# Kernel tuning notes

Measured on AMD Instinct MI355X. Metric: run time of the kernel, lower is better.

## Reference

```python
import jax, jax.numpy as jnp
import numpy as np

B, IN, H, T = 4096, 1024, 1024, 12
TIME_PENALTY = 0.01
PONDER_EPS = 0.01


def lstm_cell(x, h, c, Wih, Whh, bih, bhh):
    # PyTorch LSTMCell: gates ordered i, f, g, o
    g = x @ Wih.T + bih + h @ Whh.T + bhh  # [B, 4H]
    i, f, gg, o = jnp.split(g, 4, axis=1)
    i = jax.nn.sigmoid(i)
    f = jax.nn.sigmoid(f)
    gg = jnp.tanh(gg)
    o = jax.nn.sigmoid(o)
    c_new = f * c + i * gg
    h_new = o * jnp.tanh(c_new)
    return h_new, c_new


def setup_inputs() -> dict:
    key = jax.random.key(0)
    ks = jax.random.split(key, 12)
    k1 = 1.0 / np.sqrt(H)
    u = lambda k, shape: jax.random.uniform(k, shape, jnp.float32, -k1, k1)
    return {
        "inputs": jax.random.normal(ks[0], (B, IN), jnp.float32),
        "W_ih1": u(ks[1], (4 * H, IN + 1)),
        "W_hh1": u(ks[2], (4 * H, H)),
        "b_ih1": u(ks[3], (4 * H,)),
        "b_hh1": u(ks[4], (4 * H,)),
        "W_ih2": u(ks[5], (4 * H, H)),
        "W_hh2": u(ks[6], (4 * H, H)),
        "b_ih2": u(ks[7], (4 * H,)),
        "b_hh2": u(ks[8], (4 * H,)),
        "W_halt": u(ks[9], (1, H)),
        "b_halt": jnp.full((1,), -1.0, jnp.float32),  # initial_halting_bias
    }


def reference(inputs, W_ih1, W_hh1, b_ih1, b_hh1, W_ih2, W_hh2, b_ih2, b_hh2, W_halt, b_halt):
    batch = inputs.shape[0]
    budget = jnp.float32(1.0 - PONDER_EPS)

    h1 = jnp.zeros((batch, H), jnp.float32)
    c1 = jnp.zeros((batch, H), jnp.float32)
    h2 = jnp.zeros((batch, H), jnp.float32)
    c2 = jnp.zeros((batch, H), jnp.float32)
    halt_accum = jnp.zeros((batch, 1), jnp.float32)
    acc_out = jnp.zeros((batch, H), jnp.float32)
    acc_rem = jnp.zeros((batch, 1), jnp.float32)
    ponder_steps = jnp.zeros((batch,), jnp.float32)
    cont = jnp.ones((batch, 1), bool)
    is_first = jnp.array(True)

    def step(carry, _):
        h1, c1, h2, c2, halt_accum, acc_out, acc_rem, ponder_steps, cont, is_first = carry
        active = jnp.any(cont)  # mimic torch's early break: inactive steps are no-ops
        flag = jnp.where(is_first, 1.0, 0.0) * jnp.ones((batch, 1), jnp.float32)
        x = jnp.concatenate([inputs, flag], axis=1)
        h1n, c1n = lstm_cell(x, h1, c1, W_ih1, W_hh1, b_ih1, b_hh1)
        act = jax.nn.relu(h1n)
        h2n, c2n = lstm_cell(act, h2, c2, W_ih2, W_hh2, b_ih2, b_hh2)
        step_halt = jax.nn.sigmoid(h2n @ W_halt.T + b_halt)  # [B,1]
        cont_f = cont.astype(jnp.float32)
        masked_halt = step_halt * cont_f
        halt_n = halt_accum + masked_halt
        ending = (halt_n > budget) & cont
        cont_n = cont & jnp.logical_not(ending)
        masked_rem = ending.astype(jnp.float32) * (1.0 - halt_n)
        acc_out_n = acc_out + (masked_halt + masked_rem) * h2n
        acc_rem_n = acc_rem + masked_halt
        ponder_n = ponder_steps + cont_n[:, 0].astype(jnp.float32)
        sel = lambda new, old: jnp.where(active, new, old)
        carry_n = (sel(h1n, h1), sel(c1n, c1), sel(h2n, h2), sel(c2n, c2),
                   sel(halt_n, halt_accum), sel(acc_out_n, acc_out),
                   sel(acc_rem_n, acc_rem), sel(ponder_n, ponder_steps),
                   jnp.where(active, cont_n, cont),
                   is_first & jnp.logical_not(active))
        return carry_n, None

    carry = (h1, c1, h2, c2, halt_accum, acc_out, acc_rem, ponder_steps, cont, is_first)
    carry, _ = jax.lax.scan(step, carry, None, length=T)
    h1, c1, h2, c2, halt_accum, acc_out, acc_rem, ponder_steps, cont, _ = carry

    # for-else branch: samples still continuing after time_limit get the remainder
    acc_out = acc_out + cont.astype(jnp.float32) * (1.0 - halt_accum) * h2
    ponder_cost = -1.0 * TIME_PENALTY * jnp.mean(acc_rem)
    return acc_out, h1, c1, h2, c2, ponder_cost, ponder_steps
```

## Files before the change

kernel.cpp:

```cpp
#include <hip/hip_runtime.h>
#include <cstdint>
#include <cstddef>


typedef _Float16 f16;
typedef f16   f16x8 __attribute__((ext_vector_type(8)));
typedef f16   f16x4 __attribute__((ext_vector_type(4)));
typedef float f32x4 __attribute__((ext_vector_type(4)));

#define TSTEPS 12

#define O_ACC   0u
#define O_H1    4194304u
#define O_C1    8388608u
#define O_H2    12582912u
#define O_C2    16777216u
#define O_PCOST 20971520u
#define O_PSTEP 20971521u
#define DO_W1HI (16u<<20)
#define DO_W1LO (24u<<20)
#define DO_W2HI (32u<<20)
#define DO_W2LO (40u<<20)
#define DO_W3HI (48u<<20)
#define DO_W3LO (56u<<20)
#define DO_XHI  (64u<<20)
#define DO_XLO  (72u<<20)

#define WS_C1    (size_t)(0u)
#define WS_C2    ((size_t)16u<<20)
#define WS_H1HI0 ((size_t)32u<<20)
#define WS_H1HI1 ((size_t)40u<<20)
#define WS_H1LO0 ((size_t)48u<<20)
#define WS_H1LO1 ((size_t)56u<<20)
#define WS_H2HI0 ((size_t)64u<<20)
#define WS_H2HI1 ((size_t)72u<<20)
#define WS_H2LO0 ((size_t)80u<<20)
#define WS_H2LO1 ((size_t)88u<<20)
#define WS_ACTHI ((size_t)96u<<20)
#define WS_ACTLO ((size_t)104u<<20)
#define WS_MISC  ((size_t)112u<<20)

#define OFF_AHI 0
#define OFF_ALO 16384
#define OFF_BHI 32768
#define OFF_BLO 49152

__device__ __forceinline__ float sigmoidf_(float x) { return 1.0f / (1.0f + expf(-x)); }

__device__ __forceinline__ void glds16(const void* g, void* l) {
    __builtin_amdgcn_global_load_lds(
        (const __attribute__((address_space(1))) unsigned int*)g,
        (__attribute__((address_space(3))) unsigned int*)l, 16, 0, 0);
}

__device__ __forceinline__ void tile_compute(char* sm, f32x4 (&acc)[4][4],
                                             int wr0, int cs, int l15, int lk)
{
#pragma unroll
    for (int ks = 0; ks < 2; ++ks) {
        f16x8 ah[4], al[4];
#pragma unroll
        for (int mf = 0; mf < 4; ++mf) {
            const int row = wr0 + mf * 16 + l15;
            const int off = row * 128 + ((((ks << 2) + lk) ^ (row & 7)) << 4);
            ah[mf] = *(const f16x8*)(sm + OFF_AHI + off);
            al[mf] = *(const f16x8*)(sm + OFF_ALO + off);
        }
#pragma unroll
        for (int g = 0; g < 4; ++g) {
            const int lv  = cs * 64 + g * 16 + l15;
            const int off = lv * 128 + ((((ks << 2) + lk) ^ (lv & 7)) << 4);
            const f16x8 bh = *(const f16x8*)(sm + OFF_BHI + off);
            const f16x8 bl = *(const f16x8*)(sm + OFF_BLO + off);
#pragma unroll
            for (int mf = 0; mf < 4; ++mf) {
                acc[mf][g] = __builtin_amdgcn_mfma_f32_16x16x32_f16(ah[mf], bh, acc[mf][g], 0, 0, 0);
                acc[mf][g] = __builtin_amdgcn_mfma_f32_16x16x32_f16(ah[mf], bl, acc[mf][g], 0, 0, 0);
                acc[mf][g] = __builtin_amdgcn_mfma_f32_16x16x32_f16(al[mf], bh, acc[mf][g], 0, 0, 0);
            }
        }
    }
}

__device__ __forceinline__ void pass_glds(
    const f16* __restrict__ Ahi, const f16* __restrict__ Alo,
    const f16* __restrict__ Bhi, const f16* __restrict__ Blo,
    int m0, int hc0, f32x4 (&acc)[4][4], char* sm, bool first)
{
    const int tid = threadIdx.x, lane = tid & 63, wid = tid >> 6;
    const int wr0 = (wid >> 1) * 64, cs = wid & 1, l15 = lane & 15, lk = lane >> 4;
    const int rl = lane >> 3, sl = lane & 7;
    const int swz = (sl ^ rl) << 3;

    const f16* gsrc;
    int lbase;
    if (wid == 0)      { gsrc = Ahi + (size_t)(m0 + rl) * 1024 + swz; lbase = OFF_AHI; }
    else if (wid == 1) { gsrc = Alo + (size_t)(m0 + rl) * 1024 + swz; lbase = OFF_ALO; }
    else if (wid == 2) { gsrc = Bhi + (size_t)(hc0 + rl) * 1024 + swz; lbase = OFF_BHI; }
    else               { gsrc = Blo + (size_t)(hc0 + rl) * 1024 + swz; lbase = OFF_BLO; }

    for (int kt = 0; kt < 16; ++kt) {
        if (!first || kt) __syncthreads();
        const f16* g = gsrc + kt * 64;
        if (wid < 2) {
#pragma unroll
            for (int i = 0; i < 16; ++i)
                glds16(g + (size_t)i * 8192, sm + lbase + i * 1024);
        } else {
#pragma unroll
            for (int i = 0; i < 16; ++i) {
                const size_t rowoff =
                    (size_t)(((i >> 1) & 3) * 1024 + (i >> 3) * 16 + (i & 1) * 8) * 1024;
                glds16(g + rowoff, sm + lbase + i * 1024);
            }
        }
        __syncthreads();
        tile_compute(sm, acc, wr0, cs, l15, lk);
    }
}

__device__ __forceinline__ void pass_mixed(
    const f16* __restrict__ Ahi, const f16* __restrict__ Alo,
    const float* __restrict__ Bw,
    int m0, int hc0, f32x4 (&acc)[4][4], char* sm, bool first)
{
    const int tid = threadIdx.x, lane = tid & 63, wid = tid >> 6;
    const int wr0 = (wid >> 1) * 64, cs = wid & 1, l15 = lane & 15, lk = lane >> 4;
    const int rl = lane >> 3, sl = lane & 7;
    const int swz = (sl ^ rl) << 3;
    const f16* gsrc = (wid == 0 ? Ahi : Alo) + (size_t)(m0 + rl) * 1024 + swz;
    const int lbase = (wid == 0) ? OFF_AHI : OFF_ALO;

    const int blv = tid >> 1, bkh = (tid & 1) << 5;
    const int brow = ((blv >> 4) & 3) * 1024 + hc0 + (blv >> 6) * 16 + (blv & 15);
    const float* bsrc = Bw + (size_t)brow * 1024 + bkh;

    float4 bv[8];
    auto loadB = [&](int kt) {
#pragma unroll
        for (int i = 0; i < 8; ++i) bv[i] = *(const float4*)(bsrc + kt * 64 + i * 4);
    };
    auto writeB = [&]() {
#pragma unroll
        for (int i = 0; i < 8; ++i) {
            const float4 v = bv[i];
            const f16 s0 = (f16)v.x, s1 = (f16)v.y, s2 = (f16)v.z, s3 = (f16)v.w;
            const f16x4 hv = {s0, s1, s2, s3};
            const f16x4 lw = {(f16)(v.x - (float)s0), (f16)(v.y - (float)s1),
                              (f16)(v.z - (float)s2), (f16)(v.w - (float)s3)};
            const int kslot = (tid & 1) * 4 + (i >> 1);
            const int off = blv * 128 + ((kslot ^ (blv & 7)) << 4) + (i & 1) * 8;
            *(f16x4*)(sm + OFF_BHI + off) = hv;
            *(f16x4*)(sm + OFF_BLO + off) = lw;
        }
    };

    loadB(0);
    for (int kt = 0; kt < 16; ++kt) {
        if (!first || kt) __syncthreads();
        if (wid < 2) {
            const f16* g = gsrc + kt * 64;
#pragma unroll
            for (int i = 0; i < 16; ++i)
                glds16(g + (size_t)i * 8192, sm + lbase + i * 1024);
        }
        writeB();
        __syncthreads();
        if (kt < 15) loadB(kt + 1);
        tile_compute(sm, acc, wr0, cs, l15, lk);
    }
}

__device__ __forceinline__ void block_tile(int& m0, int& hc0) {
    const int bid = blockIdx.x;
    const int lid = (bid & 7) * 128 + (bid >> 3);
    m0  = (lid & 31) * 128;
    hc0 = (lid >> 5) * 32;
}

__global__ __launch_bounds__(256) void k_stepA(
    const f16* __restrict__ xhi, const f16* __restrict__ xlo,
    const f16* __restrict__ W1hi, const f16* __restrict__ W1lo,
    const float* __restrict__ Whh1,
    const f16* __restrict__ h1hi_in, const f16* __restrict__ h1lo_in,
    const float* __restrict__ bih1, const float* __restrict__ bhh1,
    const float* __restrict__ flagcol,
    float* __restrict__ c1,
    f16* __restrict__ h1hi_out, f16* __restrict__ h1lo_out,
    f16* __restrict__ acthi, f16* __restrict__ actlo,
    const unsigned* __restrict__ cnt_prev, int step)
{
    if (step > 0 && cnt_prev[0] == 0u) return;
    __shared__ __align__(16) char sm[65536];
    int m0, hc0; block_tile(m0, hc0);
    f32x4 acc[4][4];
#pragma unroll
    for (int a = 0; a < 4; ++a)
#pragma unroll
        for (int b = 0; b < 4; ++b) acc[a][b] = (f32x4){0.f, 0.f, 0.f, 0.f};

    pass_glds(xhi, xlo, W1hi, W1lo, m0, hc0, acc, sm, true);
    if (step > 0)
        pass_mixed(h1hi_in, h1lo_in, Whh1, m0, hc0, acc, sm, false);

    const int tid = threadIdx.x, lane = tid & 63, wid = tid >> 6;
    const int wr0 = (wid >> 1) * 64, cs = wid & 1, l15 = lane & 15, lk = lane >> 4;
#pragma unroll
    for (int mf = 0; mf < 4; ++mf)
#pragma unroll
        for (int r = 0; r < 4; ++r) {
            const int row = m0 + wr0 + mf * 16 + lk * 4 + r;
            const int hc  = hc0 + cs * 16 + l15;
            float p[4];
#pragma unroll
            for (int g = 0; g < 4; ++g) {
                const int R = g * 1024 + hc;
                p[g] = acc[mf][g][r] + bih1[R] + bhh1[R];
                if (step == 0) p[g] += flagcol[R];
            }
            const float ig = sigmoidf_(p[0]);
            const float fg = sigmoidf_(p[1]);
            const float gg = tanhf(p[2]);
            const float og = sigmoidf_(p[3]);
            const int idx = row * 1024 + hc;
            const float cn = fg * c1[idx] + ig * gg;
            c1[idx] = cn;
            const float h = og * tanhf(cn);
            const f16 hh = (f16)h;
            const f16 hl = (f16)(h - (float)hh);
            h1hi_out[idx] = hh; h1lo_out[idx] = hl;
            const bool pos = h > 0.0f;
            acthi[idx] = pos ? hh : (f16)0.0f;
            actlo[idx] = pos ? hl : (f16)0.0f;
        }
}

__global__ __launch_bounds__(256) void k_stepB(
    const f16* __restrict__ acthi, const f16* __restrict__ actlo,
    const f16* __restrict__ W2hi, const f16* __restrict__ W2lo,
    const f16* __restrict__ h2hi_in, const f16* __restrict__ h2lo_in,
    const f16* __restrict__ W3hi, const f16* __restrict__ W3lo,
    const float* __restrict__ bih2, const float* __restrict__ bhh2,
    float* __restrict__ c2, f16* __restrict__ h2hi_out, f16* __restrict__ h2lo_out,
    const unsigned* __restrict__ cnt_prev, int step)
{
    if (step > 0 && cnt_prev[0] == 0u) return;
    __shared__ __align__(16) char sm[65536];
    int m0, hc0; block_tile(m0, hc0);
    f32x4 acc[4][4];
#pragma unroll
    for (int a = 0; a < 4; ++a)
#pragma unroll
        for (int b = 0; b < 4; ++b) acc[a][b] = (f32x4){0.f, 0.f, 0.f, 0.f};

    pass_glds(acthi, actlo, W2hi, W2lo, m0, hc0, acc, sm, true);
    if (step > 0)
        pass_glds(h2hi_in, h2lo_in, W3hi, W3lo, m0, hc0, acc, sm, false);

    const int tid = threadIdx.x, lane = tid & 63, wid = tid >> 6;
    const int wr0 = (wid >> 1) * 64, cs = wid & 1, l15 = lane & 15, lk = lane >> 4;
#pragma unroll
    for (int mf = 0; mf < 4; ++mf)
#pragma unroll
        for (int r = 0; r < 4; ++r) {
            const int row = m0 + wr0 + mf * 16 + lk * 4 + r;
            const int hc  = hc0 + cs * 16 + l15;
            float p[4];
#pragma unroll
            for (int g = 0; g < 4; ++g) {
                const int R = g * 1024 + hc;
                p[g] = acc[mf][g][r] + bih2[R] + bhh2[R];
            }
            const float ig = sigmoidf_(p[0]);
            const float fg = sigmoidf_(p[1]);
            const float gg = tanhf(p[2]);
            const float og = sigmoidf_(p[3]);
            const int idx = row * 1024 + hc;
            const float cn = fg * c2[idx] + ig * gg;
            c2[idx] = cn;
            const float h = og * tanhf(cn);
            const f16 hh = (f16)h;
            h2hi_out[idx] = hh;
            h2lo_out[idx] = (f16)(h - (float)hh);
        }
}

__global__ __launch_bounds__(256) void k_halt(
    const f16* __restrict__ h2hi, const f16* __restrict__ h2lo,
    const float* __restrict__ Whalt, const float* __restrict__ bhalt,
    float* __restrict__ halt, float* __restrict__ cont, float* __restrict__ coef,
    float* __restrict__ ponder_out, unsigned* __restrict__ ctrl,
    const unsigned* __restrict__ cnt_prev, int step)
{
    if (step > 0 && cnt_prev[0] == 0u) return;
    const int lane = threadIdx.x & 63;
    const int b = blockIdx.x * 4 + (threadIdx.x >> 6);
    const size_t base = (size_t)b * 1024;
    float sum = 0.0f;
    for (int k = lane; k < 1024; k += 64)
        sum += ((float)h2hi[base + k] + (float)h2lo[base + k]) * Whalt[k];
#pragma unroll
    for (int off = 32; off > 0; off >>= 1) sum += __shfl_down(sum, off, 64);
    if (lane == 0) {
        const float sh = sigmoidf_(sum + bhalt[0]);
        float co = 0.0f;
        if (cont[b] != 0.0f) {
            const float hn = halt[b] + sh;
            const bool ending = hn > 0.99f;
            co = sh + (ending ? (1.0f - hn) : 0.0f);
            halt[b] = hn;
            if (!ending) {
                ponder_out[b] += 1.0f;
                atomicAdd(&ctrl[step], 1u);
            } else {
                cont[b] = 0.0f;
            }
        }
        coef[b] = co;
        if (b == 0) ctrl[12] = (unsigned)(step + 1);
    }
}

__global__ __launch_bounds__(256) void k_accum(
    const f16* __restrict__ h2hi, const f16* __restrict__ h2lo,
    const float* __restrict__ coef, float* __restrict__ acc_out,
    const unsigned* __restrict__ cnt_prev, int step)
{
    if (step > 0 && cnt_prev[0] == 0u) return;
    const int b = blockIdx.x;
    const float co = coef[b];
    if (co == 0.0f) return;
    const size_t base = (size_t)b * 1024;
    const int i = threadIdx.x;
    const f16x4 hv = *(const f16x4*)(h2hi + base + i * 4);
    const f16x4 lv = *(const f16x4*)(h2lo + base + i * 4);
    float4* dst = (float4*)(acc_out + base);
    float4 d = dst[i];
    d.x = fmaf(co, (float)hv[0] + (float)lv[0], d.x);
    d.y = fmaf(co, (float)hv[1] + (float)lv[1], d.y);
    d.z = fmaf(co, (float)hv[2] + (float)lv[2], d.z);
    d.w = fmaf(co, (float)hv[3] + (float)lv[3], d.w);
    dst[i] = d;
}

__global__ __launch_bounds__(256) void k_small_init(
    float* __restrict__ halt, float* __restrict__ cont,
    float* __restrict__ ponder_out, unsigned* __restrict__ ctrl)
{
    const int b = blockIdx.x * 256 + threadIdx.x;
    if (b < 4096) { halt[b] = 0.0f; cont[b] = 1.0f; ponder_out[b] = 0.0f; }
    if (b < 16) ctrl[b] = 0u;
}

__global__ __launch_bounds__(256) void k_split_flat(
    const float* __restrict__ src, f16* __restrict__ hi, f16* __restrict__ lo)
{
    const size_t i = ((size_t)blockIdx.x * 256 + threadIdx.x) * 4;
    const float4 v = *(const float4*)(src + i);
    const f16 s0 = (f16)v.x, s1 = (f16)v.y, s2 = (f16)v.z, s3 = (f16)v.w;
    const f16x4 hv = {s0, s1, s2, s3};
    const f16x4 lw = {(f16)(v.x - (float)s0), (f16)(v.y - (float)s1),
                      (f16)(v.z - (float)s2), (f16)(v.w - (float)s3)};
    *(f16x4*)(hi + i) = hv;
    *(f16x4*)(lo + i) = lw;
}

__global__ __launch_bounds__(256) void k_split_wih1(
    const float* __restrict__ src, f16* __restrict__ hi, f16* __restrict__ lo,
    float* __restrict__ flagcol)
{
    const int t = blockIdx.x * 256 + threadIdx.x;
    const int row = t >> 8, c4 = (t & 255) << 2;
    const float* s = src + (size_t)row * 1025 + c4;
    const float v0 = s[0], v1 = s[1], v2 = s[2], v3 = s[3];
    const f16 s0 = (f16)v0, s1 = (f16)v1, s2 = (f16)v2, s3 = (f16)v3;
    const f16x4 hv = {s0, s1, s2, s3};
    const f16x4 lw = {(f16)(v0 - (float)s0), (f16)(v1 - (float)s1),
                      (f16)(v2 - (float)s2), (f16)(v3 - (float)s3)};
    const size_t di = (size_t)row * 1024 + c4;
    *(f16x4*)(hi + di) = hv;
    *(f16x4*)(lo + di) = lw;
    if ((t & 255) == 0) flagcol[row] = src[(size_t)row * 1025 + 1024];
}

__global__ __launch_bounds__(256) void k_fin1(
    const f16* __restrict__ h1hi0, const f16* __restrict__ h1hi1,
    const f16* __restrict__ h1lo0, const f16* __restrict__ h1lo1,
    const f16* __restrict__ h2hi0, const f16* __restrict__ h2hi1,
    const f16* __restrict__ h2lo0, const f16* __restrict__ h2lo1,
    const float* __restrict__ c1s, const float* __restrict__ c2s,
    const float* __restrict__ halt, const float* __restrict__ cont,
    const unsigned* __restrict__ ctrl, float* __restrict__ out)
{
    const int par = (int)(ctrl[12] & 1u);
    const f16* h1h = par ? h1hi1 : h1hi0;
    const f16* h1l = par ? h1lo1 : h1lo0;
    const f16* h2h = par ? h2hi1 : h2hi0;
    const f16* h2l = par ? h2lo1 : h2lo0;
    const int b = blockIdx.x;
    const float rem = (cont[b] != 0.0f) ? (1.0f - halt[b]) : 0.0f;
    const int base = b * 1024;
    for (int i = threadIdx.x; i < 1024; i += 256) {
        const float h1v = (float)h1h[base + i] + (float)h1l[base + i];
        const float h2v = (float)h2h[base + i] + (float)h2l[base + i];
        out[O_H1 + base + i] = h1v;
        out[O_C1 + base + i] = c1s[base + i];
        out[O_H2 + base + i] = h2v;
        out[O_C2 + base + i] = c2s[base + i];
        if (rem != 0.0f) out[O_ACC + base + i] += rem * h2v;
    }
}

__global__ __launch_bounds__(256) void k_fin2(
    const float* __restrict__ halt, float* __restrict__ out)
{
    __shared__ float red[256];
    float s = 0.0f;
    for (int i = threadIdx.x; i < 4096; i += 256) s += halt[i];
    red[threadIdx.x] = s;
    __syncthreads();
    for (int w = 128; w > 0; w >>= 1) {
        if (threadIdx.x < w) red[threadIdx.x] += red[threadIdx.x + w];
        __syncthreads();
    }
    if (threadIdx.x == 0) out[O_PCOST] = -0.01f * (red[0] * (1.0f / 4096.0f));
}

extern "C" void kernel_launch(void* const* d_in, const int* in_sizes, int n_in,
                              void* d_out, int out_size, void* d_ws, size_t ws_size,
                              hipStream_t stream) {
    const float* inputs = (const float*)d_in[0];
    const float* W_ih1  = (const float*)d_in[1];
    const float* W_hh1  = (const float*)d_in[2];
    const float* b_ih1  = (const float*)d_in[3];
    const float* b_hh1  = (const float*)d_in[4];
    const float* W_ih2  = (const float*)d_in[5];
    const float* W_hh2  = (const float*)d_in[6];
    const float* b_ih2  = (const float*)d_in[7];
    const float* b_hh2  = (const float*)d_in[8];
    const float* W_halt = (const float*)d_in[9];
    const float* b_halt = (const float*)d_in[10];

    float* out = (float*)d_out;
    char*  ob  = (char*)d_out;
    f16* W1hi = (f16*)(ob + DO_W1HI); f16* W1lo = (f16*)(ob + DO_W1LO);
    f16* W2hi = (f16*)(ob + DO_W2HI); f16* W2lo = (f16*)(ob + DO_W2LO);
    f16* W3hi = (f16*)(ob + DO_W3HI); f16* W3lo = (f16*)(ob + DO_W3LO);
    f16* xhi  = (f16*)(ob + DO_XHI);  f16* xlo  = (f16*)(ob + DO_XLO);

    char* wsb = (char*)d_ws;
    float* c1s = (float*)(wsb + WS_C1);
    float* c2s = (float*)(wsb + WS_C2);
    f16* h1hi[2] = { (f16*)(wsb + WS_H1HI0), (f16*)(wsb + WS_H1HI1) };
    f16* h1lo[2] = { (f16*)(wsb + WS_H1LO0), (f16*)(wsb + WS_H1LO1) };
    f16* h2hi[2] = { (f16*)(wsb + WS_H2HI0), (f16*)(wsb + WS_H2HI1) };
    f16* h2lo[2] = { (f16*)(wsb + WS_H2LO0), (f16*)(wsb + WS_H2LO1) };
    f16* acthi   = (f16*)(wsb + WS_ACTHI);
    f16* actlo   = (f16*)(wsb + WS_ACTLO);
    float* halt    = (float*)(wsb + WS_MISC);
    float* cont    = halt + 4096;
    float* coef    = cont + 4096;
    float* flagcol = coef + 4096;
    unsigned* ctrl = (unsigned*)(flagcol + 4096);

    const size_t mb16 = (size_t)4096 * 1024 * sizeof(float);
    hipMemsetAsync(out + O_ACC, 0, mb16, stream);
    hipMemsetAsync(c1s, 0, mb16, stream);
    hipMemsetAsync(c2s, 0, mb16, stream);
    k_small_init<<<16, 256, 0, stream>>>(halt, cont, out + O_PSTEP, ctrl);

    k_split_wih1<<<4096, 256, 0, stream>>>(W_ih1, W1hi, W1lo, flagcol);
    k_split_flat<<<4096, 256, 0, stream>>>(W_ih2, W2hi, W2lo);
    k_split_flat<<<4096, 256, 0, stream>>>(W_hh2, W3hi, W3lo);
    k_split_flat<<<4096, 256, 0, stream>>>(inputs, xhi, xlo);

    for (int s = 0; s < TSTEPS; ++s) {
        const int wsel = (s & 1) ? 0 : 1;
        const int rsel = 1 - wsel;
        const unsigned* cnt_prev = ctrl + (s > 0 ? s - 1 : 0);

        k_stepA<<<1024, 256, 0, stream>>>(xhi, xlo, W1hi, W1lo, W_hh1,
                                          h1hi[rsel], h1lo[rsel],
                                          b_ih1, b_hh1, flagcol, c1s,
                                          h1hi[wsel], h1lo[wsel], acthi, actlo,
                                          cnt_prev, s);
        k_stepB<<<1024, 256, 0, stream>>>(acthi, actlo, W2hi, W2lo,
                                          h2hi[rsel], h2lo[rsel], W3hi, W3lo,
                                          b_ih2, b_hh2, c2s,
                                          h2hi[wsel], h2lo[wsel],
                                          cnt_prev, s);
        k_halt<<<1024, 256, 0, stream>>>(h2hi[wsel], h2lo[wsel], W_halt, b_halt,
                                         halt, cont, coef, out + O_PSTEP, ctrl,
                                         cnt_prev, s);
        k_accum<<<4096, 256, 0, stream>>>(h2hi[wsel], h2lo[wsel], coef,
                                          out + O_ACC, cnt_prev, s);
    }

    k_fin1<<<4096, 256, 0, stream>>>(h1hi[0], h1hi[1], h1lo[0], h1lo[1],
                                     h2hi[0], h2hi[1], h2lo[0], h2lo[1],
                                     c1s, c2s, halt, cont, ctrl, out);
    k_fin2<<<1, 256, 0, stream>>>(halt, out);
}
```

Baseline: 1.636 ms.

## Hoist input projection out of recurrence and enlarge double-buffered GEMM tiles

The x·W_ih1 product does not change across time steps, so it is now computed once into a Z1 buffer (with biases folded in) before the loop, and each step only adds the recurrent h·W_hh1 term. The GEMM tiles grow from 128x32 to 256x64 per block with 512 threads and a double-buffered LDS pipeline that prefetches the next K-slice while MFMAs run. Weights W_ih2 and W_hh2 are now split to hi/lo fp16 inside the kernel from fp32 rather than by separate pre-pass kernels. The trade-offs are 128KB of LDS per block, fewer blocks (256), more register pressure from the 8x4 accumulators, and reuse of output and workspace buffers as scratch for Z1 and the split x/W1.

```diff
diff --git a/kernel.cpp b/kernel.cpp
--- a/kernel.cpp
+++ b/kernel.cpp
@@ -17,14 +17,6 @@
 #define O_C2    16777216u
 #define O_PCOST 20971520u
 #define O_PSTEP 20971521u
-#define DO_W1HI (16u<<20)
-#define DO_W1LO (24u<<20)
-#define DO_W2HI (32u<<20)
-#define DO_W2LO (40u<<20)
-#define DO_W3HI (48u<<20)
-#define DO_W3LO (56u<<20)
-#define DO_XHI  (64u<<20)
-#define DO_XLO  (72u<<20)
 
 #define WS_C1    (size_t)(0u)
 #define WS_C2    ((size_t)16u<<20)
@@ -40,10 +32,11 @@
 #define WS_ACTLO ((size_t)104u<<20)
 #define WS_MISC  ((size_t)112u<<20)
 
-#define OFF_AHI 0
-#define OFF_ALO 16384
-#define OFF_BHI 32768
-#define OFF_BLO 49152
+#define SEC_AHI 0
+#define SEC_ALO 16384
+#define SEC_BHI 32768
+#define SEC_BLO 49152
+#define BUFSZ   65536
 
 __device__ __forceinline__ float sigmoidf_(float x) { return 1.0f / (1.0f + expf(-x)); }
 
@@ -53,169 +46,214 @@
         (__attribute__((address_space(3))) unsigned int*)l, 16, 0, 0);
 }
 
-__device__ __forceinline__ void tile_compute(char* sm, f32x4 (&acc)[4][4],
-                                             int wr0, int cs, int l15, int lk)
-{
-#pragma unroll
-    for (int ks = 0; ks < 2; ++ks) {
-        f16x8 ah[4], al[4];
-#pragma unroll
-        for (int mf = 0; mf < 4; ++mf) {
-            const int row = wr0 + mf * 16 + l15;
-            const int off = row * 128 + ((((ks << 2) + lk) ^ (row & 7)) << 4);
-            ah[mf] = *(const f16x8*)(sm + OFF_AHI + off);
-            al[mf] = *(const f16x8*)(sm + OFF_ALO + off);
-        }
-#pragma unroll
-        for (int g = 0; g < 4; ++g) {
-            const int lv  = cs * 64 + g * 16 + l15;
-            const int off = lv * 128 + ((((ks << 2) + lk) ^ (lv & 7)) << 4);
-            const f16x8 bh = *(const f16x8*)(sm + OFF_BHI + off);
-            const f16x8 bl = *(const f16x8*)(sm + OFF_BLO + off);
-#pragma unroll
-            for (int mf = 0; mf < 4; ++mf) {
-                acc[mf][g] = __builtin_amdgcn_mfma_f32_16x16x32_f16(ah[mf], bh, acc[mf][g], 0, 0, 0);
-                acc[mf][g] = __builtin_amdgcn_mfma_f32_16x16x32_f16(ah[mf], bl, acc[mf][g], 0, 0, 0);
-                acc[mf][g] = __builtin_amdgcn_mfma_f32_16x16x32_f16(al[mf], bh, acc[mf][g], 0, 0, 0);
-            }
-        }
-    }
-}
-
-__device__ __forceinline__ void pass_glds(
+__device__ __forceinline__ void block_tile(int& m0, int& hc0) {
+    const int bid = blockIdx.x;
+    const int lid = (bid & 7) * 32 + (bid >> 3);
+    m0  = (lid & 15) * 256;
+    hc0 = (lid >> 4) * 64;
+}
+
+template<bool B_PAIR>
+__device__ __forceinline__ void pass256(
     const f16* __restrict__ Ahi, const f16* __restrict__ Alo,
     const f16* __restrict__ Bhi, const f16* __restrict__ Blo,
-    int m0, int hc0, f32x4 (&acc)[4][4], char* sm, bool first)
+    const float* __restrict__ Bf32,
+    int m0, int hc0, f32x4 (&acc)[8][4], char* sm)
 {
     const int tid = threadIdx.x, lane = tid & 63, wid = tid >> 6;
-    const int wr0 = (wid >> 1) * 64, cs = wid & 1, l15 = lane & 15, lk = lane >> 4;
-    const int rl = lane >> 3, sl = lane & 7;
-    const int swz = (sl ^ rl) << 3;
-
-    const f16* gsrc;
-    int lbase;
-    if (wid == 0)      { gsrc = Ahi + (size_t)(m0 + rl) * 1024 + swz; lbase = OFF_AHI; }
-    else if (wid == 1) { gsrc = Alo + (size_t)(m0 + rl) * 1024 + swz; lbase = OFF_ALO; }
-    else if (wid == 2) { gsrc = Bhi + (size_t)(hc0 + rl) * 1024 + swz; lbase = OFF_BHI; }
-    else               { gsrc = Blo + (size_t)(hc0 + rl) * 1024 + swz; lbase = OFF_BLO; }
-
-    for (int kt = 0; kt < 16; ++kt) {
-        if (!first || kt) __syncthreads();
-        const f16* g = gsrc + kt * 64;
-        if (wid < 2) {
-#pragma unroll
-            for (int i = 0; i < 16; ++i)
-                glds16(g + (size_t)i * 8192, sm + lbase + i * 1024);
-        } else {
-#pragma unroll
-            for (int i = 0; i < 16; ++i) {
-                const size_t rowoff =
-                    (size_t)(((i >> 1) & 3) * 1024 + (i >> 3) * 16 + (i & 1) * 8) * 1024;
-                glds16(g + rowoff, sm + lbase + i * 1024);
-            }
-        }
-        __syncthreads();
-        tile_compute(sm, acc, wr0, cs, l15, lk);
-    }
-}
-
-__device__ __forceinline__ void pass_mixed(
-    const f16* __restrict__ Ahi, const f16* __restrict__ Alo,
-    const float* __restrict__ Bw,
-    int m0, int hc0, f32x4 (&acc)[4][4], char* sm, bool first)
-{
-    const int tid = threadIdx.x, lane = tid & 63, wid = tid >> 6;
-    const int wr0 = (wid >> 1) * 64, cs = wid & 1, l15 = lane & 15, lk = lane >> 4;
-    const int rl = lane >> 3, sl = lane & 7;
-    const int swz = (sl ^ rl) << 3;
-    const f16* gsrc = (wid == 0 ? Ahi : Alo) + (size_t)(m0 + rl) * 1024 + swz;
-    const int lbase = (wid == 0) ? OFF_AHI : OFF_ALO;
-
-    const int blv = tid >> 1, bkh = (tid & 1) << 5;
-    const int brow = ((blv >> 4) & 3) * 1024 + hc0 + (blv >> 6) * 16 + (blv & 15);
-    const float* bsrc = Bw + (size_t)brow * 1024 + bkh;
-
-    float4 bv[8];
+    const int wm  = (wid >> 2) * 128;
+    const int wnb = wid & 3;
+    const int l15 = lane & 15, lk = lane >> 4;
+    const int rswz16 = (lk ^ (l15 & 3)) << 4;
+
+    int aoff[8], boff[4];
+#pragma unroll
+    for (int mf = 0; mf < 8; ++mf) aoff[mf] = (wm + mf * 16 + l15) * 64 + rswz16;
+#pragma unroll
+    for (int nf = 0; nf < 4; ++nf) boff[nf] = (wnb * 64 + nf * 16 + l15) * 64 + rswz16;
+
+    constexpr int NOPS = B_PAIR ? 8 : 4;
+    const f16* gsrc[NOPS];
+    int ldst[NOPS];
+    {
+        const int gl_d = lane >> 2;
+        const int swzel = ((lane & 3) ^ (gl_d & 3)) * 8;
+#pragma unroll
+        for (int i = 0; i < NOPS; ++i) {
+            const int o = wid * NOPS + i;
+            const int sec = o >> 4, j = o & 15;
+            const f16* base;
+            size_t row;
+            if (sec <= 1) { base = (sec == 0) ? Ahi : Alo; row = (size_t)(m0 + 16 * j + gl_d); }
+            else {
+                base = (sec == 2) ? Bhi : Blo;
+                row = (size_t)((j & 3) * 1024 + hc0 + (j >> 2) * 16 + gl_d);
+            }
+            gsrc[i] = base + row * 1024 + swzel;
+            ldst[i] = sec * 16384 + j * 1024 + lane * 16;
+        }
+    }
+
+    const int blv = tid >> 1;
+    const float* bsrc = nullptr;
+    float4 breg[4];
+    if constexpr (!B_PAIR) {
+        const int wrow = ((blv >> 4) & 3) * 1024 + hc0 + (blv >> 6) * 16 + (blv & 15);
+        bsrc = Bf32 + (size_t)wrow * 1024 + (tid & 1) * 16;
+    }
+
+    auto issue = [&](int i, int kt, char* buf) {
+        glds16(gsrc[i] + kt * 32, buf + ldst[i]);
+    };
     auto loadB = [&](int kt) {
 #pragma unroll
-        for (int i = 0; i < 8; ++i) bv[i] = *(const float4*)(bsrc + kt * 64 + i * 4);
+        for (int i = 0; i < 4; ++i) breg[i] = *(const float4*)(bsrc + kt * 32 + i * 4);
     };
-    auto writeB = [&]() {
-#pragma unroll
-        for (int i = 0; i < 8; ++i) {
-            const float4 v = bv[i];
+    auto writeB = [&](char* buf) {
+#pragma unroll
+        for (int i = 0; i < 4; ++i) {
+            const float4 v = breg[i];
             const f16 s0 = (f16)v.x, s1 = (f16)v.y, s2 = (f16)v.z, s3 = (f16)v.w;
             const f16x4 hv = {s0, s1, s2, s3};
             const f16x4 lw = {(f16)(v.x - (float)s0), (f16)(v.y - (float)s1),
                               (f16)(v.z - (float)s2), (f16)(v.w - (float)s3)};
-            const int kslot = (tid & 1) * 4 + (i >> 1);
-            const int off = blv * 128 + ((kslot ^ (blv & 7)) << 4) + (i & 1) * 8;
-            *(f16x4*)(sm + OFF_BHI + off) = hv;
-            *(f16x4*)(sm + OFF_BLO + off) = lw;
+            const int s = (((tid & 1) * 2 + (i >> 1)) ^ (blv & 3));
+            const int off = blv * 64 + (s << 4) + (i & 1) * 8;
+            *(f16x4*)(buf + SEC_BHI + off) = hv;
+            *(f16x4*)(buf + SEC_BLO + off) = lw;
         }
     };
 
-    loadB(0);
-    for (int kt = 0; kt < 16; ++kt) {
-        if (!first || kt) __syncthreads();
-        if (wid < 2) {
-            const f16* g = gsrc + kt * 64;
-#pragma unroll
-            for (int i = 0; i < 16; ++i)
-                glds16(g + (size_t)i * 8192, sm + lbase + i * 1024);
-        }
-        writeB();
-        __syncthreads();
-        if (kt < 15) loadB(kt + 1);
-        tile_compute(sm, acc, wr0, cs, l15, lk);
-    }
-}
-
-__device__ __forceinline__ void block_tile(int& m0, int& hc0) {
-    const int bid = blockIdx.x;
-    const int lid = (bid & 7) * 128 + (bid >> 3);
-    m0  = (lid & 31) * 128;
-    hc0 = (lid >> 5) * 32;
-}
-
-__global__ __launch_bounds__(256) void k_stepA(
+    constexpr int IST_P[5] = {0, 3, 6, 8, 8};
+    constexpr int IST_M[5] = {0, 2, 3, 4, 4};
+
+#pragma unroll
+    for (int i = 0; i < NOPS; ++i) issue(i, 0, sm);
+    if constexpr (!B_PAIR) {
+        loadB(0);
+        asm volatile("s_waitcnt vmcnt(0)" ::: "memory");
+        writeB(sm);
+    }
+    asm volatile("s_waitcnt vmcnt(0) lgkmcnt(0)" ::: "memory");
+    __builtin_amdgcn_s_barrier();
+    asm volatile("" ::: "memory");
+
+    int cur = 0;
+#pragma unroll 1
+    for (int kt = 0; kt < 32; ++kt) {
+        char* bc = sm + cur * BUFSZ;
+        char* bn = sm + (cur ^ 1) * BUFSZ;
+        const bool pre = (kt < 31);
+        f16x8 bh[4], bl[4];
+#pragma unroll
+        for (int p = 0; p < 4; ++p) {
+            f16x8 ah0 = *(const f16x8*)(bc + SEC_AHI + aoff[2 * p]);
+            f16x8 ah1 = *(const f16x8*)(bc + SEC_AHI + aoff[2 * p + 1]);
+            f16x8 al0 = *(const f16x8*)(bc + SEC_ALO + aoff[2 * p]);
+            f16x8 al1 = *(const f16x8*)(bc + SEC_ALO + aoff[2 * p + 1]);
+            if (p == 0) {
+#pragma unroll
+                for (int nf = 0; nf < 4; ++nf) {
+                    bh[nf] = *(const f16x8*)(bc + SEC_BHI + boff[nf]);
+                    bl[nf] = *(const f16x8*)(bc + SEC_BLO + boff[nf]);
+                }
+            }
+            if (pre) {
+                if constexpr (B_PAIR) {
+#pragma unroll
+                    for (int i = IST_P[p]; i < IST_P[p + 1]; ++i) issue(i, kt + 1, bn);
+                } else {
+#pragma unroll
+                    for (int i = IST_M[p]; i < IST_M[p + 1]; ++i) issue(i, kt + 1, bn);
+                    if (p == 0) loadB(kt + 1);
+                }
+            }
+            __builtin_amdgcn_s_barrier();
+#pragma unroll
+            for (int i = 0; i < 2; ++i) {
+                const f16x8 xh = i ? ah1 : ah0;
+                const f16x8 xl = i ? al1 : al0;
+#pragma unroll
+                for (int nf = 0; nf < 4; ++nf) {
+                    acc[2 * p + i][nf] = __builtin_amdgcn_mfma_f32_16x16x32_f16(xh, bh[nf], acc[2 * p + i][nf], 0, 0, 0);
+                    acc[2 * p + i][nf] = __builtin_amdgcn_mfma_f32_16x16x32_f16(xh, bl[nf], acc[2 * p + i][nf], 0, 0, 0);
+                    acc[2 * p + i][nf] = __builtin_amdgcn_mfma_f32_16x16x32_f16(xl, bh[nf], acc[2 * p + i][nf], 0, 0, 0);
+                }
+            }
+            if (p < 3) __builtin_amdgcn_s_barrier();
+        }
+        asm volatile("s_waitcnt vmcnt(0)" ::: "memory");
+        if constexpr (!B_PAIR) { if (pre) writeB(bn); }
+        asm volatile("s_waitcnt lgkmcnt(0)" ::: "memory");
+        __builtin_amdgcn_s_barrier();
+        asm volatile("" ::: "memory");
+        cur ^= 1;
+    }
+}
+
+__global__ __launch_bounds__(512) void k_z1(
     const f16* __restrict__ xhi, const f16* __restrict__ xlo,
     const f16* __restrict__ W1hi, const f16* __restrict__ W1lo,
-    const float* __restrict__ Whh1,
+    const float* __restrict__ bih1, const float* __restrict__ bhh1,
+    float* __restrict__ Z1)
+{
+    __shared__ __align__(16) char sm[2 * BUFSZ];
+    int m0, hc0; block_tile(m0, hc0);
+    f32x4 acc[8][4];
+#pragma unroll
+    for (int a = 0; a < 8; ++a)
+#pragma unroll
+        for (int b = 0; b < 4; ++b) acc[a][b] = (f32x4){0.f, 0.f, 0.f, 0.f};
+    pass256<true>(xhi, xlo, W1hi, W1lo, nullptr, m0, hc0, acc, sm);
+
+    const int tid = threadIdx.x, lane = tid & 63, wid = tid >> 6;
+    const int wm = (wid >> 2) * 128, wnb = wid & 3, l15 = lane & 15, lk = lane >> 4;
+    const int hc = hc0 + wnb * 16 + l15;
+#pragma unroll
+    for (int mf = 0; mf < 8; ++mf)
+#pragma unroll
+        for (int r = 0; r < 4; ++r) {
+            const int row = m0 + wm + mf * 16 + lk * 4 + r;
+#pragma unroll
+            for (int g = 0; g < 4; ++g) {
+                const int R = g * 1024 + hc;
+                Z1[(size_t)row * 4096 + R] = acc[mf][g][r] + bih1[R] + bhh1[R];
+            }
+        }
+}
+
+__global__ __launch_bounds__(512) void k_stepA(
+    const float* __restrict__ Z1, const float* __restrict__ Whh1,
     const f16* __restrict__ h1hi_in, const f16* __restrict__ h1lo_in,
-    const float* __restrict__ bih1, const float* __restrict__ bhh1,
-    const float* __restrict__ flagcol,
-    float* __restrict__ c1,
+    const float* __restrict__ flagcol, float* __restrict__ c1,
     f16* __restrict__ h1hi_out, f16* __restrict__ h1lo_out,
     f16* __restrict__ acthi, f16* __restrict__ actlo,
     const unsigned* __restrict__ cnt_prev, int step)
 {
     if (step > 0 && cnt_prev[0] == 0u) return;
-    __shared__ __align__(16) char sm[65536];
+    __shared__ __align__(16) char sm[2 * BUFSZ];
     int m0, hc0; block_tile(m0, hc0);
-    f32x4 acc[4][4];
-#pragma unroll
-    for (int a = 0; a < 4; ++a)
+    f32x4 acc[8][4];
+#pragma unroll
+    for (int a = 0; a < 8; ++a)
 #pragma unroll
         for (int b = 0; b < 4; ++b) acc[a][b] = (f32x4){0.f, 0.f, 0.f, 0.f};
-
-    pass_glds(xhi, xlo, W1hi, W1lo, m0, hc0, acc, sm, true);
     if (step > 0)
-        pass_mixed(h1hi_in, h1lo_in, Whh1, m0, hc0, acc, sm, false);
+        pass256<false>(h1hi_in, h1lo_in, nullptr, nullptr, Whh1, m0, hc0, acc, sm);
 
     const int tid = threadIdx.x, lane = tid & 63, wid = tid >> 6;
-    const int wr0 = (wid >> 1) * 64, cs = wid & 1, l15 = lane & 15, lk = lane >> 4;
-#pragma unroll
-    for (int mf = 0; mf < 4; ++mf)
+    const int wm = (wid >> 2) * 128, wnb = wid & 3, l15 = lane & 15, lk = lane >> 4;
+    const int hc = hc0 + wnb * 16 + l15;
+#pragma unroll
+    for (int mf = 0; mf < 8; ++mf)
 #pragma unroll
         for (int r = 0; r < 4; ++r) {
-            const int row = m0 + wr0 + mf * 16 + lk * 4 + r;
-            const int hc  = hc0 + cs * 16 + l15;
+            const int row = m0 + wm + mf * 16 + lk * 4 + r;
             float p[4];
 #pragma unroll
             for (int g = 0; g < 4; ++g) {
                 const int R = g * 1024 + hc;
-                p[g] = acc[mf][g][r] + bih1[R] + bhh1[R];
+                p[g] = acc[mf][g][r] + Z1[(size_t)row * 4096 + R];
                 if (step == 0) p[g] += flagcol[R];
             }
             const float ig = sigmoidf_(p[0]);
@@ -235,36 +273,35 @@
         }
 }
 
-__global__ __launch_bounds__(256) void k_stepB(
+__global__ __launch_bounds__(512) void k_stepB(
     const f16* __restrict__ acthi, const f16* __restrict__ actlo,
-    const f16* __restrict__ W2hi, const f16* __restrict__ W2lo,
+    const float* __restrict__ Wih2,
     const f16* __restrict__ h2hi_in, const f16* __restrict__ h2lo_in,
-    const f16* __restrict__ W3hi, const f16* __restrict__ W3lo,
+    const float* __restrict__ Whh2,
     const float* __restrict__ bih2, const float* __restrict__ bhh2,
     float* __restrict__ c2, f16* __restrict__ h2hi_out, f16* __restrict__ h2lo_out,
     const unsigned* __restrict__ cnt_prev, int step)
 {
     if (step > 0 && cnt_prev[0] == 0u) return;
-    __shared__ __align__(16) char sm[65536];
+    __shared__ __align__(16) char sm[2 * BUFSZ];
     int m0, hc0; block_tile(m0, hc0);
-    f32x4 acc[4][4];
-#pragma unroll
-    for (int a = 0; a < 4; ++a)
+    f32x4 acc[8][4];
+#pragma unroll
+    for (int a = 0; a < 8; ++a)
 #pragma unroll
         for (int b = 0; b < 4; ++b) acc[a][b] = (f32x4){0.f, 0.f, 0.f, 0.f};
-
-    pass_glds(acthi, actlo, W2hi, W2lo, m0, hc0, acc, sm, true);
+    pass256<false>(acthi, actlo, nullptr, nullptr, Wih2, m0, hc0, acc, sm);
     if (step > 0)
-        pass_glds(h2hi_in, h2lo_in, W3hi, W3lo, m0, hc0, acc, sm, false);
+        pass256<false>(h2hi_in, h2lo_in, nullptr, nullptr, Whh2, m0, hc0, acc, sm);
 
     const int tid = threadIdx.x, lane = tid & 63, wid = tid >> 6;
-    const int wr0 = (wid >> 1) * 64, cs = wid & 1, l15 = lane & 15, lk = lane >> 4;
-#pragma unroll
-    for (int mf = 0; mf < 4; ++mf)
+    const int wm = (wid >> 2) * 128, wnb = wid & 3, l15 = lane & 15, lk = lane >> 4;
+    const int hc = hc0 + wnb * 16 + l15;
+#pragma unroll
+    for (int mf = 0; mf < 8; ++mf)
 #pragma unroll
         for (int r = 0; r < 4; ++r) {
-            const int row = m0 + wr0 + mf * 16 + lk * 4 + r;
-            const int hc  = hc0 + cs * 16 + l15;
+            const int row = m0 + wm + mf * 16 + lk * 4 + r;
             float p[4];
 #pragma unroll
             for (int g = 0; g < 4; ++g) {
@@ -442,11 +479,7 @@
     const float* b_halt = (const float*)d_in[10];
 
     float* out = (float*)d_out;
-    char*  ob  = (char*)d_out;
-    f16* W1hi = (f16*)(ob + DO_W1HI); f16* W1lo = (f16*)(ob + DO_W1LO);
-    f16* W2hi = (f16*)(ob + DO_W2HI); f16* W2lo = (f16*)(ob + DO_W2LO);
-    f16* W3hi = (f16*)(ob + DO_W3HI); f16* W3lo = (f16*)(ob + DO_W3LO);
-    f16* xhi  = (f16*)(ob + DO_XHI);  f16* xlo  = (f16*)(ob + DO_XLO);
+    float* Z1  = out + O_H1;
 
     char* wsb = (char*)d_ws;
     float* c1s = (float*)(wsb + WS_C1);
@@ -463,6 +496,9 @@
     float* flagcol = coef + 4096;
     unsigned* ctrl = (unsigned*)(flagcol + 4096);
 
+    f16* xhi  = h1hi[0]; f16* xlo  = h1lo[0];
+    f16* W1hi = h2hi[0]; f16* W1lo = h2lo[0];
+
     const size_t mb16 = (size_t)4096 * 1024 * sizeof(float);
     hipMemsetAsync(out + O_ACC, 0, mb16, stream);
     hipMemsetAsync(c1s, 0, mb16, stream);
@@ -470,25 +506,23 @@
     k_small_init<<<16, 256, 0, stream>>>(halt, cont, out + O_PSTEP, ctrl);
 
     k_split_wih1<<<4096, 256, 0, stream>>>(W_ih1, W1hi, W1lo, flagcol);
-    k_split_flat<<<4096, 256, 0, stream>>>(W_ih2, W2hi, W2lo);
-    k_split_flat<<<4096, 256, 0, stream>>>(W_hh2, W3hi, W3lo);
     k_split_flat<<<4096, 256, 0, stream>>>(inputs, xhi, xlo);
+    k_z1<<<256, 512, 0, stream>>>(xhi, xlo, W1hi, W1lo, b_ih1, b_hh1, Z1);
 
     for (int s = 0; s < TSTEPS; ++s) {
         const int wsel = (s & 1) ? 0 : 1;
         const int rsel = 1 - wsel;
         const unsigned* cnt_prev = ctrl + (s > 0 ? s - 1 : 0);
 
-        k_stepA<<<1024, 256, 0, stream>>>(xhi, xlo, W1hi, W1lo, W_hh1,
-                                          h1hi[rsel], h1lo[rsel],
-                                          b_ih1, b_hh1, flagcol, c1s,
-                                          h1hi[wsel], h1lo[wsel], acthi, actlo,
-                                          cnt_prev, s);
-        k_stepB<<<1024, 256, 0, stream>>>(acthi, actlo, W2hi, W2lo,
-                                          h2hi[rsel], h2lo[rsel], W3hi, W3lo,
-                                          b_ih2, b_hh2, c2s,
-                                          h2hi[wsel], h2lo[wsel],
-                                          cnt_prev, s);
+        k_stepA<<<256, 512, 0, stream>>>(Z1, W_hh1, h1hi[rsel], h1lo[rsel],
+                                         flagcol, c1s,
+                                         h1hi[wsel], h1lo[wsel], acthi, actlo,
+                                         cnt_prev, s);
+        k_stepB<<<256, 512, 0, stream>>>(acthi, actlo, W_ih2,
+                                         h2hi[rsel], h2lo[rsel], W_hh2,
+                                         b_ih2, b_hh2, c2s,
+                                         h2hi[wsel], h2lo[wsel],
+                                         cnt_prev, s);
         k_halt<<<1024, 256, 0, stream>>>(h2hi[wsel], h2lo[wsel], W_halt, b_halt,
                                          halt, cont, coef, out + O_PSTEP, ctrl,
                                          cnt_prev, s);
```

After: 1.483 ms. 1.1x faster.
